# Kernel tuning notes

Measured on AMD Instinct MI355X. Metric: run time of the kernel, lower is better.

The kernel has to match this reference:

```python
import jax, jax.numpy as jnp
import numpy as np

NUM_HEADS = 12
DIM = 768
HEAD_DIM = DIM // NUM_HEADS


def setup_inputs() -> dict:
    key = jax.random.key(0)
    k1, k2, k3, k4 = jax.random.split(key, 4)
    B, N, C = 4, 8192, DIM
    x = jax.random.normal(k1, (B, N, C), dtype=jnp.float32)
    # torch nn.Linear stores weight as (out_features, in_features)
    W_qkv = jax.random.normal(k2, (3 * C, C), dtype=jnp.float32) * (1.0 / np.sqrt(C))
    W_proj = jax.random.normal(k3, (C, C), dtype=jnp.float32) * (1.0 / np.sqrt(C))
    b_proj = jax.random.normal(k4, (C,), dtype=jnp.float32) * 0.01
    return {"x": x, "W_qkv": W_qkv, "W_proj": W_proj, "b_proj": b_proj}


def reference(x, W_qkv, W_proj, b_proj):
    B, N, C = x.shape
    H, D = NUM_HEADS, HEAD_DIM
    qkv = x @ W_qkv.T                                  # [B,N,3C]
    qkv = qkv.reshape(B, N, 3, H, D).transpose(2, 0, 3, 1, 4)  # [3,B,H,N,D]
    q, k, v = qkv[0], qkv[1], qkv[2]
    q = jax.nn.elu(q) + 1.0
    k = jax.nn.elu(k) + 1.0
    k_sum = k.sum(axis=-2)                             # [B,H,D]
    kv = jnp.einsum('bhnd,bhne->bhde', k, v)           # [B,H,D,D]
    numerator = jnp.einsum('bhnd,bhde->bhne', q, kv)   # [B,H,N,D]
    denominator = jnp.einsum('bhnd,bhd->bhn', q, k_sum)
    out = numerator / (denominator[..., None] + 1e-6)
    out = out.transpose(0, 2, 1, 3).reshape(B, N, C)   # [B,N,C]
    out = out @ W_proj.T + b_proj
    return out
```

## Files before the change

kernel.cpp:

```cpp
#include <hip/hip_runtime.h>
#include <hip/hip_bf16.h>
#include <stdint.h>

typedef __attribute__((ext_vector_type(8))) short short8;
typedef __attribute__((ext_vector_type(4))) float floatx4;

#define NB 4
#define NN 8192
#define NC 768
#define NH 12
#define ND 64
#define LDQKV 2304

__device__ __forceinline__ float bf2f(ushort u) {
    union { float f; uint32_t i; } x; x.i = ((uint32_t)u) << 16; return x.f;
}
__device__ __forceinline__ ushort f2bf(float f) {
    union { float f; uint32_t i; } x; x.f = f;
    uint32_t r = x.i + 0x7fff + ((x.i >> 16) & 1);
    return (ushort)(r >> 16);
}
typedef const __attribute__((address_space(1))) uint32_t* gas1_t;
typedef __attribute__((address_space(3))) uint32_t* las3_t;
__device__ __forceinline__ void gl_lds16(const void* g, const void* l) {
    __builtin_amdgcn_global_load_lds((gas1_t)(uintptr_t)g,
                                     (las3_t)(uint32_t)(uintptr_t)l, 16, 0, 0);
}

__global__ __launch_bounds__(256) void cvt_bf16(const float* __restrict__ src,
                                                ushort* __restrict__ dst, int n) {
    const int i = (blockIdx.x * 256 + threadIdx.x) * 8;
    if (i >= n) return;
    const float4 a = *(const float4*)(src + i);
    const float4 b = *(const float4*)(src + i + 4);
    short8 v;
    v[0] = (short)f2bf(a.x); v[1] = (short)f2bf(a.y);
    v[2] = (short)f2bf(a.z); v[3] = (short)f2bf(a.w);
    v[4] = (short)f2bf(b.x); v[5] = (short)f2bf(b.y);
    v[6] = (short)f2bf(b.z); v[7] = (short)f2bf(b.w);
    *(short8*)(dst + i) = v;
}


__device__ __forceinline__ void stage_half(const ushort* __restrict__ src, int row0,
                                           int k0, int K, ushort* dst, int t, int w) {
    const int rsub = t >> 3;
    const int ch = (t & 7) ^ (rsub & 7);
    const ushort* g0 = src + (size_t)(row0 + rsub) * K + k0 + ch * 8;
    gl_lds16(g0,                 dst + w * 512);
    gl_lds16(g0 + (size_t)64 * K, dst + 4096 + w * 512);
}

#define PHASE_SYNC() do {                                        \
    __builtin_amdgcn_s_barrier();                                \
    asm volatile("s_waitcnt lgkmcnt(0)" ::: "memory");           \
    __builtin_amdgcn_sched_barrier(0);                           \
} while (0)

template<int LDC, bool ELU, bool BIAS, typename OutT>
__global__ __launch_bounds__(512) void gemm256(const ushort* __restrict__ A,
                                               const ushort* __restrict__ Bw,
                                               const float* __restrict__ bias,
                                               OutT* __restrict__ Cout, int K) {
    __shared__ __align__(16) ushort SL[2][4][8192];
    const int t = threadIdx.x, w = t >> 6, lane = t & 63;
    const int l16 = lane & 15, quad = lane >> 4;
    const int wm = w >> 2, wn = w & 3;
    const int bro = (wn & 1) * 64;

    const int gx = gridDim.x;
    const int nwg = gx * gridDim.y;
    int bid = blockIdx.y * gx + blockIdx.x;
    bid = (bid & 7) * (nwg >> 3) + (bid >> 3);
    const int m0 = (bid / gx) * 256;
    const int n0 = (bid % gx) * 256;
    const int NT = K >> 6;

    floatx4 acc[8][4] = {};
    short8 af[4][2], b01[2][2], b23[2][2];

    stage_half(Bw, n0,       0,  K, &SL[0][0][0], t, w);
    stage_half(Bw, n0 + 128, 0,  K, &SL[0][1][0], t, w);
    stage_half(A,  m0,       0,  K, &SL[0][2][0], t, w);
    stage_half(A,  m0 + 128, 0,  K, &SL[0][3][0], t, w);
    stage_half(Bw, n0,       64, K, &SL[1][0][0], t, w);
    stage_half(Bw, n0 + 128, 64, K, &SL[1][1][0], t, w);
    asm volatile("s_waitcnt vmcnt(4)" ::: "memory");
    __builtin_amdgcn_s_barrier();

    for (int j = 0; j < NT; j++) {
        const int buf = j & 1;
        const ushort* As = &SL[buf][2 + wm][0];
        const ushort* Bs = &SL[buf][wn >> 1][0];

        #pragma unroll
        for (int mi = 0; mi < 4; mi++) {
            const int row = mi * 16 + l16;
            const int sw = (row & 7) << 3;
            const int base = row * 64 + quad * 8;
            af[mi][0] = *(const short8*)&As[base ^ sw];
            af[mi][1] = *(const short8*)&As[(base + 32) ^ sw];
        }
        #pragma unroll
        for (int ni = 0; ni < 2; ni++) {
            const int row = bro + ni * 16 + l16;
            const int sw = (row & 7) << 3;
            const int base = row * 64 + quad * 8;
            b01[ni][0] = *(const short8*)&Bs[base ^ sw];
            b01[ni][1] = *(const short8*)&Bs[(base + 32) ^ sw];
        }
        if (j + 1 < NT) stage_half(A, m0, (j + 1) * 64, K, &SL[buf ^ 1][2][0], t, w);
        PHASE_SYNC();
        __builtin_amdgcn_s_setprio(1);
        #pragma unroll
        for (int mi = 0; mi < 4; mi++)
            #pragma unroll
            for (int ni = 0; ni < 2; ni++) {
                acc[mi][ni] = __builtin_amdgcn_mfma_f32_16x16x32_bf16(af[mi][0], b01[ni][0], acc[mi][ni], 0, 0, 0);
                acc[mi][ni] = __builtin_amdgcn_mfma_f32_16x16x32_bf16(af[mi][1], b01[ni][1], acc[mi][ni], 0, 0, 0);
            }
        __builtin_amdgcn_s_setprio(0);
        __builtin_amdgcn_s_barrier();

        #pragma unroll
        for (int ni = 0; ni < 2; ni++) {
            const int row = bro + (2 + ni) * 16 + l16;
            const int sw = (row & 7) << 3;
            const int base = row * 64 + quad * 8;
            b23[ni][0] = *(const short8*)&Bs[base ^ sw];
            b23[ni][1] = *(const short8*)&Bs[(base + 32) ^ sw];
        }
        if (j + 1 < NT) stage_half(A, m0 + 128, (j + 1) * 64, K, &SL[buf ^ 1][3][0], t, w);
        PHASE_SYNC();
        __builtin_amdgcn_s_setprio(1);
        #pragma unroll
        for (int mi = 0; mi < 4; mi++)
            #pragma unroll
            for (int ni = 0; ni < 2; ni++) {
                acc[mi][2 + ni] = __builtin_amdgcn_mfma_f32_16x16x32_bf16(af[mi][0], b23[ni][0], acc[mi][2 + ni], 0, 0, 0);
                acc[mi][2 + ni] = __builtin_amdgcn_mfma_f32_16x16x32_bf16(af[mi][1], b23[ni][1], acc[mi][2 + ni], 0, 0, 0);
            }
        __builtin_amdgcn_s_setprio(0);
        __builtin_amdgcn_s_barrier();

        #pragma unroll
        for (int mi = 0; mi < 4; mi++) {
            const int row = (4 + mi) * 16 + l16;
            const int sw = (row & 7) << 3;
            const int base = row * 64 + quad * 8;
            af[mi][0] = *(const short8*)&As[base ^ sw];
            af[mi][1] = *(const short8*)&As[(base + 32) ^ sw];
        }
        if (j + 2 < NT) stage_half(Bw, n0, (j + 2) * 64, K, &SL[buf][0][0], t, w);
        PHASE_SYNC();
        __builtin_amdgcn_s_setprio(1);
        #pragma unroll
        for (int mi = 0; mi < 4; mi++)
            #pragma unroll
            for (int ni = 0; ni < 2; ni++) {
                acc[4 + mi][ni] = __builtin_amdgcn_mfma_f32_16x16x32_bf16(af[mi][0], b01[ni][0], acc[4 + mi][ni], 0, 0, 0);
                acc[4 + mi][ni] = __builtin_amdgcn_mfma_f32_16x16x32_bf16(af[mi][1], b01[ni][1], acc[4 + mi][ni], 0, 0, 0);
            }
        __builtin_amdgcn_s_setprio(0);
        __builtin_amdgcn_s_barrier();

        if (j + 2 < NT) stage_half(Bw, n0 + 128, (j + 2) * 64, K, &SL[buf][1][0], t, w);
        __builtin_amdgcn_s_barrier();
        __builtin_amdgcn_s_setprio(1);
        #pragma unroll
        for (int mi = 0; mi < 4; mi++)
            #pragma unroll
            for (int ni = 0; ni < 2; ni++) {
                acc[4 + mi][2 + ni] = __builtin_amdgcn_mfma_f32_16x16x32_bf16(af[mi][0], b23[ni][0], acc[4 + mi][2 + ni], 0, 0, 0);
                acc[4 + mi][2 + ni] = __builtin_amdgcn_mfma_f32_16x16x32_bf16(af[mi][1], b23[ni][1], acc[4 + mi][2 + ni], 0, 0, 0);
            }
        __builtin_amdgcn_s_setprio(0);
        if (j < NT - 2) asm volatile("s_waitcnt vmcnt(4)" ::: "memory");
        else            asm volatile("s_waitcnt vmcnt(0)" ::: "memory");
        __builtin_amdgcn_s_barrier();
    }

    #pragma unroll
    for (int mi = 0; mi < 8; mi++) {
        const int row = m0 + wm * 128 + mi * 16 + quad * 4;
        #pragma unroll
        for (int n = 0; n < 4; n++) {
            const int col = n0 + wn * 64 + n * 16 + l16;
            float bval = 0.f;
            if (BIAS) bval = bias[col];
            #pragma unroll
            for (int r = 0; r < 4; r++) {
                float v = acc[mi][n][r];
                if (ELU) { if (col < 2 * NC) v = (v > 0.f) ? v + 1.f : __expf(v); }
                if (BIAS) v += bval;
                if (sizeof(OutT) == 2) Cout[(size_t)(row + r) * LDC + col] = (OutT)f2bf(v);
                else                   Cout[(size_t)(row + r) * LDC + col] = (OutT)v;
            }
        }
    }
}

__global__ __launch_bounds__(256) void kv_ksum(const ushort* __restrict__ qkv,
                                               float* __restrict__ kvws,
                                               float* __restrict__ ksws) {
    __shared__ ushort klds[128 * 64];
    __shared__ ushort vlds[128 * 64];
    __shared__ float  kvred[64 * 64];
    __shared__ float  ksred[4][64];
    const int bh = blockIdx.y, b = bh / NH, h = bh % NH;
    const int t = threadIdx.x, w = t >> 6, lane = t & 63, l16 = lane & 15, quad = lane >> 4;
    const int n0 = blockIdx.x * 1024;
    const ushort* kbase = qkv + (size_t)(b * NN) * LDQKV + NC     + h * ND;
    const ushort* vbase = qkv + (size_t)(b * NN) * LDQKV + 2 * NC + h * ND;

    floatx4 acc[4][4] = {};
    float ksp = 0.f;
    const int rowT = t >> 3, ch = t & 7;

    for (int s = 0; s < 8; s++) {
        const int nb = n0 + s * 128;
        #pragma unroll
        for (int i = 0; i < 4; i++) {
            const size_t r = (size_t)(nb + i * 32 + rowT) * LDQKV + ch * 8;
            gl_lds16(kbase + r, klds + i * 2048 + w * 512);
            gl_lds16(vbase + r, vlds + i * 2048 + w * 512);
        }
        __syncthreads();
        short8 af[4], bfr[4];
        #pragma unroll
        for (int dt = 0; dt < 4; dt++) {
            short8 v;
            #pragma unroll
            for (int j = 0; j < 8; j++)
                v[j] = (short)klds[(w * 32 + quad * 8 + j) * 64 + dt * 16 + l16];
            af[dt] = v;
        }
        #pragma unroll
        for (int et = 0; et < 4; et++) {
            short8 v;
            #pragma unroll
            for (int j = 0; j < 8; j++)
                v[j] = (short)vlds[(w * 32 + quad * 8 + j) * 64 + et * 16 + l16];
            bfr[et] = v;
        }
        #pragma unroll
        for (int dt = 0; dt < 4; dt++)
            #pragma unroll
            for (int et = 0; et < 4; et++)
                acc[dt][et] = __builtin_amdgcn_mfma_f32_16x16x32_bf16(af[dt], bfr[et], acc[dt][et], 0, 0, 0);
        #pragma unroll
        for (int n = 0; n < 32; n++) ksp += bf2f(klds[(w * 32 + n) * 64 + lane]);
        __syncthreads();
    }

    if (w == 0) {
        #pragma unroll
        for (int dt = 0; dt < 4; dt++)
            #pragma unroll
            for (int et = 0; et < 4; et++)
                #pragma unroll
                for (int r = 0; r < 4; r++)
                    kvred[(dt * 16 + quad * 4 + r) * 64 + et * 16 + l16] = acc[dt][et][r];
    }
    ksred[w][lane] = ksp;
    __syncthreads();
    if (w != 0) {
        #pragma unroll
        for (int dt = 0; dt < 4; dt++)
            #pragma unroll
            for (int et = 0; et < 4; et++)
                #pragma unroll
                for (int r = 0; r < 4; r++)
                    atomicAdd(&kvred[(dt * 16 + quad * 4 + r) * 64 + et * 16 + l16], acc[dt][et][r]);
    }
    __syncthreads();
    for (int i = t; i < 4096; i += 256) atomicAdd(&kvws[(size_t)bh * 4096 + i], kvred[i]);
    if (t < 64) atomicAdd(&ksws[bh * 64 + t], ksred[0][t] + ksred[1][t] + ksred[2][t] + ksred[3][t]);
}

__global__ __launch_bounds__(256) void attn_apply(const ushort* __restrict__ qkv,
                                                  const float* __restrict__ kvws,
                                                  const float* __restrict__ ksws,
                                                  ushort* __restrict__ outpre) {
    __shared__ ushort kvb[64 * 80];
    const int bh = blockIdx.y, b = bh / NH, h = bh % NH;
    const int t = threadIdx.x, w = t >> 6, lane = t & 63, l16 = lane & 15, quad = lane >> 4;

    for (int i = t; i < 4096; i += 256) {
        const int d = i >> 6, e = i & 63;
        kvb[d * 80 + e] = f2bf(kvws[(size_t)bh * 4096 + i]);
    }
    for (int i = t; i < 1024; i += 256) {
        const int d = i >> 4, c = i & 15;
        kvb[d * 80 + 64 + c] = (c == 0) ? f2bf(ksws[bh * 64 + d]) : (ushort)0;
    }
    __syncthreads();

    short8 bfr[5][2];
    #pragma unroll
    for (int et = 0; et < 5; et++)
        #pragma unroll
        for (int ks = 0; ks < 2; ks++) {
            short8 v;
            #pragma unroll
            for (int j = 0; j < 8; j++)
                v[j] = (short)kvb[(ks * 32 + quad * 8 + j) * 80 + et * 16 + l16];
            bfr[et][ks] = v;
        }

    const ushort* qbase = qkv + (size_t)(b * NN) * LDQKV + h * ND;
    ushort* obase = outpre + (size_t)(b * NN) * NC + h * ND;
    const int n0 = blockIdx.x * 1024;

    for (int it = 0; it < 16; it++) {
        const int nt = n0 + (it * 4 + w) * 16;
        const ushort* qp = qbase + (size_t)(nt + l16) * LDQKV + quad * 8;
        const short8 a0 = *(const short8*)qp;
        const short8 a1 = *(const short8*)(qp + 32);
        floatx4 acc[5] = {};
        #pragma unroll
        for (int et = 0; et < 5; et++) {
            acc[et] = __builtin_amdgcn_mfma_f32_16x16x32_bf16(a0, bfr[et][0], acc[et], 0, 0, 0);
            acc[et] = __builtin_amdgcn_mfma_f32_16x16x32_bf16(a1, bfr[et][1], acc[et], 0, 0, 0);
        }
        float dv[4];
        #pragma unroll
        for (int r = 0; r < 4; r++) dv[r] = __shfl(acc[4][r], lane & 48);
        #pragma unroll
        for (int et = 0; et < 4; et++)
            #pragma unroll
            for (int r = 0; r < 4; r++) {
                const float o = acc[et][r] / (dv[r] + 1e-6f);
                obase[(size_t)(nt + quad * 4 + r) * NC + et * 16 + l16] = f2bf(o);
            }
    }
}

__global__ void zero_f32(float* p, int n) {
    const int i = blockIdx.x * 256 + threadIdx.x;
    if (i < n) p[i] = 0.f;
}

extern "C" void kernel_launch(void* const* d_in, const int* in_sizes, int n_in,
                              void* d_out, int out_size, void* d_ws, size_t ws_size,
                              hipStream_t stream) {
    (void)in_sizes; (void)n_in; (void)out_size; (void)ws_size;
    const float* X     = (const float*)d_in[0];
    const float* Wqkv  = (const float*)d_in[1];
    const float* Wproj = (const float*)d_in[2];
    const float* bproj = (const float*)d_in[3];
    float* out = (float*)d_out;

    char* ws = (char*)d_ws;
    size_t off = 0;
    ushort* qkv     = (ushort*)(ws + off); off += (size_t)32768 * 2304 * 2;
    ushort* outpre  = (ushort*)(ws + off); off += (size_t)32768 * 768 * 2;
    ushort* xbf     = (ushort*)(ws + off); off += (size_t)32768 * 768 * 2;
    ushort* wqkvbf  = (ushort*)(ws + off); off += (size_t)2304 * 768 * 2;
    ushort* wprojbf = (ushort*)(ws + off); off += (size_t)768 * 768 * 2;
    float*  kvws    = (float*)(ws + off);  off += (size_t)48 * 4096 * 4;
    float*  ksws    = (float*)(ws + off);

    const int nx = 32768 * 768, nwq = 2304 * 768, nwp = 768 * 768;
    cvt_bf16<<<nx  / (256 * 8), 256, 0, stream>>>(X,     xbf,     nx);
    cvt_bf16<<<nwq / (256 * 8), 256, 0, stream>>>(Wqkv,  wqkvbf,  nwq);
    cvt_bf16<<<nwp / (256 * 8), 256, 0, stream>>>(Wproj, wprojbf, nwp);

    const int nzero = 48 * 4096 + 48 * 64;
    zero_f32<<<(nzero + 255) / 256, 256, 0, stream>>>(kvws, nzero);

    gemm256<LDQKV, true, false, ushort><<<dim3(9, 128), 512, 0, stream>>>(xbf, wqkvbf, nullptr, qkv, NC);
    kv_ksum<<<dim3(8, 48), 256, 0, stream>>>(qkv, kvws, ksws);
    attn_apply<<<dim3(8, 48), 256, 0, stream>>>(qkv, kvws, ksws, outpre);
    gemm256<NC, false, true, float><<<dim3(3, 128), 512, 0, stream>>>(outpre, wprojbf, bproj, out, NC);
}
```

Baseline: 465.2 us.

## Restructure GEMM phase pipeline and replace atomic KV reduction with partials

```diff
diff --git a/kernel.cpp b/kernel.cpp
--- a/kernel.cpp
+++ b/kernel.cpp
@@ -51,12 +51,6 @@
     gl_lds16(g0 + (size_t)64 * K, dst + 4096 + w * 512);
 }
 
-#define PHASE_SYNC() do {                                        \
-    __builtin_amdgcn_s_barrier();                                \
-    asm volatile("s_waitcnt lgkmcnt(0)" ::: "memory");           \
-    __builtin_amdgcn_sched_barrier(0);                           \
-} while (0)
-
 template<int LDC, bool ELU, bool BIAS, typename OutT>
 __global__ __launch_bounds__(512) void gemm256(const ushort* __restrict__ A,
                                                const ushort* __restrict__ Bw,
@@ -77,7 +71,6 @@
     const int NT = K >> 6;
 
     floatx4 acc[8][4] = {};
-    short8 af[4][2], b01[2][2], b23[2][2];
 
     stage_half(Bw, n0,       0,  K, &SL[0][0][0], t, w);
     stage_half(Bw, n0 + 128, 0,  K, &SL[0][1][0], t, w);
@@ -92,14 +85,15 @@
         const int buf = j & 1;
         const ushort* As = &SL[buf][2 + wm][0];
         const ushort* Bs = &SL[buf][wn >> 1][0];
+        short8 afl[4][2], afh[4][2], b01[2][2], b23[2][2];
 
         #pragma unroll
         for (int mi = 0; mi < 4; mi++) {
             const int row = mi * 16 + l16;
             const int sw = (row & 7) << 3;
             const int base = row * 64 + quad * 8;
-            af[mi][0] = *(const short8*)&As[base ^ sw];
-            af[mi][1] = *(const short8*)&As[(base + 32) ^ sw];
+            afl[mi][0] = *(const short8*)&As[base ^ sw];
+            afl[mi][1] = *(const short8*)&As[(base + 32) ^ sw];
         }
         #pragma unroll
         for (int ni = 0; ni < 2; ni++) {
@@ -109,19 +103,6 @@
             b01[ni][0] = *(const short8*)&Bs[base ^ sw];
             b01[ni][1] = *(const short8*)&Bs[(base + 32) ^ sw];
         }
-        if (j + 1 < NT) stage_half(A, m0, (j + 1) * 64, K, &SL[buf ^ 1][2][0], t, w);
-        PHASE_SYNC();
-        __builtin_amdgcn_s_setprio(1);
-        #pragma unroll
-        for (int mi = 0; mi < 4; mi++)
-            #pragma unroll
-            for (int ni = 0; ni < 2; ni++) {
-                acc[mi][ni] = __builtin_amdgcn_mfma_f32_16x16x32_bf16(af[mi][0], b01[ni][0], acc[mi][ni], 0, 0, 0);
-                acc[mi][ni] = __builtin_amdgcn_mfma_f32_16x16x32_bf16(af[mi][1], b01[ni][1], acc[mi][ni], 0, 0, 0);
-            }
-        __builtin_amdgcn_s_setprio(0);
-        __builtin_amdgcn_s_barrier();
-
         #pragma unroll
         for (int ni = 0; ni < 2; ni++) {
             const int row = bro + (2 + ni) * 16 + l16;
@@ -130,15 +111,15 @@
             b23[ni][0] = *(const short8*)&Bs[base ^ sw];
             b23[ni][1] = *(const short8*)&Bs[(base + 32) ^ sw];
         }
-        if (j + 1 < NT) stage_half(A, m0 + 128, (j + 1) * 64, K, &SL[buf ^ 1][3][0], t, w);
-        PHASE_SYNC();
+
+        if (j + 1 < NT) stage_half(A, m0, (j + 1) * 64, K, &SL[buf ^ 1][2][0], t, w);
         __builtin_amdgcn_s_setprio(1);
         #pragma unroll
         for (int mi = 0; mi < 4; mi++)
             #pragma unroll
             for (int ni = 0; ni < 2; ni++) {
-                acc[mi][2 + ni] = __builtin_amdgcn_mfma_f32_16x16x32_bf16(af[mi][0], b23[ni][0], acc[mi][2 + ni], 0, 0, 0);
-                acc[mi][2 + ni] = __builtin_amdgcn_mfma_f32_16x16x32_bf16(af[mi][1], b23[ni][1], acc[mi][2 + ni], 0, 0, 0);
+                acc[mi][ni] = __builtin_amdgcn_mfma_f32_16x16x32_bf16(afl[mi][0], b01[ni][0], acc[mi][ni], 0, 0, 0);
+                acc[mi][ni] = __builtin_amdgcn_mfma_f32_16x16x32_bf16(afl[mi][1], b01[ni][1], acc[mi][ni], 0, 0, 0);
             }
         __builtin_amdgcn_s_setprio(0);
         __builtin_amdgcn_s_barrier();
@@ -148,31 +129,41 @@
             const int row = (4 + mi) * 16 + l16;
             const int sw = (row & 7) << 3;
             const int base = row * 64 + quad * 8;
-            af[mi][0] = *(const short8*)&As[base ^ sw];
-            af[mi][1] = *(const short8*)&As[(base + 32) ^ sw];
-        }
-        if (j + 2 < NT) stage_half(Bw, n0, (j + 2) * 64, K, &SL[buf][0][0], t, w);
-        PHASE_SYNC();
+            afh[mi][0] = *(const short8*)&As[base ^ sw];
+            afh[mi][1] = *(const short8*)&As[(base + 32) ^ sw];
+        }
+        if (j + 1 < NT) stage_half(A, m0 + 128, (j + 1) * 64, K, &SL[buf ^ 1][3][0], t, w);
         __builtin_amdgcn_s_setprio(1);
         #pragma unroll
         for (int mi = 0; mi < 4; mi++)
             #pragma unroll
             for (int ni = 0; ni < 2; ni++) {
-                acc[4 + mi][ni] = __builtin_amdgcn_mfma_f32_16x16x32_bf16(af[mi][0], b01[ni][0], acc[4 + mi][ni], 0, 0, 0);
-                acc[4 + mi][ni] = __builtin_amdgcn_mfma_f32_16x16x32_bf16(af[mi][1], b01[ni][1], acc[4 + mi][ni], 0, 0, 0);
+                acc[mi][2 + ni] = __builtin_amdgcn_mfma_f32_16x16x32_bf16(afl[mi][0], b23[ni][0], acc[mi][2 + ni], 0, 0, 0);
+                acc[mi][2 + ni] = __builtin_amdgcn_mfma_f32_16x16x32_bf16(afl[mi][1], b23[ni][1], acc[mi][2 + ni], 0, 0, 0);
             }
         __builtin_amdgcn_s_setprio(0);
         __builtin_amdgcn_s_barrier();
 
+        if (j + 2 < NT) stage_half(Bw, n0, (j + 2) * 64, K, &SL[buf][0][0], t, w);
+        __builtin_amdgcn_s_setprio(1);
+        #pragma unroll
+        for (int mi = 0; mi < 4; mi++)
+            #pragma unroll
+            for (int ni = 0; ni < 2; ni++) {
+                acc[4 + mi][ni] = __builtin_amdgcn_mfma_f32_16x16x32_bf16(afh[mi][0], b01[ni][0], acc[4 + mi][ni], 0, 0, 0);
+                acc[4 + mi][ni] = __builtin_amdgcn_mfma_f32_16x16x32_bf16(afh[mi][1], b01[ni][1], acc[4 + mi][ni], 0, 0, 0);
+            }
+        __builtin_amdgcn_s_setprio(0);
+        __builtin_amdgcn_s_barrier();
+
         if (j + 2 < NT) stage_half(Bw, n0 + 128, (j + 2) * 64, K, &SL[buf][1][0], t, w);
-        __builtin_amdgcn_s_barrier();
         __builtin_amdgcn_s_setprio(1);
         #pragma unroll
         for (int mi = 0; mi < 4; mi++)
             #pragma unroll
             for (int ni = 0; ni < 2; ni++) {
-                acc[4 + mi][2 + ni] = __builtin_amdgcn_mfma_f32_16x16x32_bf16(af[mi][0], b23[ni][0], acc[4 + mi][2 + ni], 0, 0, 0);
-                acc[4 + mi][2 + ni] = __builtin_amdgcn_mfma_f32_16x16x32_bf16(af[mi][1], b23[ni][1], acc[4 + mi][2 + ni], 0, 0, 0);
+                acc[4 + mi][2 + ni] = __builtin_amdgcn_mfma_f32_16x16x32_bf16(afh[mi][0], b23[ni][0], acc[4 + mi][2 + ni], 0, 0, 0);
+                acc[4 + mi][2 + ni] = __builtin_amdgcn_mfma_f32_16x16x32_bf16(afh[mi][1], b23[ni][1], acc[4 + mi][2 + ni], 0, 0, 0);
             }
         __builtin_amdgcn_s_setprio(0);
         if (j < NT - 2) asm volatile("s_waitcnt vmcnt(4)" ::: "memory");
@@ -201,12 +192,12 @@
 }
 
 __global__ __launch_bounds__(256) void kv_ksum(const ushort* __restrict__ qkv,
-                                               float* __restrict__ kvws,
-                                               float* __restrict__ ksws) {
-    __shared__ ushort klds[128 * 64];
-    __shared__ ushort vlds[128 * 64];
-    __shared__ float  kvred[64 * 64];
+                                               float* __restrict__ kv_part,
+                                               float* __restrict__ ks_part) {
+    __shared__ ushort kvsh[2][128 * 64];
     __shared__ float  ksred[4][64];
+    ushort* klds = kvsh[0];
+    ushort* vlds = kvsh[1];
     const int bh = blockIdx.y, b = bh / NH, h = bh % NH;
     const int t = threadIdx.x, w = t >> 6, lane = t & 63, l16 = lane & 15, quad = lane >> 4;
     const int n0 = blockIdx.x * 1024;
@@ -214,7 +205,10 @@
     const ushort* vbase = qkv + (size_t)(b * NN) * LDQKV + 2 * NC + h * ND;
 
     floatx4 acc[4][4] = {};
-    float ksp = 0.f;
+    floatx4 aks[4] = {};
+    short8 bones;
+    #pragma unroll
+    for (int j = 0; j < 8; j++) bones[j] = (short)0x3F80;
     const int rowT = t >> 3, ch = t & 7;
 
     for (int s = 0; s < 8; s++) {
@@ -244,55 +238,94 @@
             bfr[et] = v;
         }
         #pragma unroll
-        for (int dt = 0; dt < 4; dt++)
+        for (int dt = 0; dt < 4; dt++) {
             #pragma unroll
             for (int et = 0; et < 4; et++)
                 acc[dt][et] = __builtin_amdgcn_mfma_f32_16x16x32_bf16(af[dt], bfr[et], acc[dt][et], 0, 0, 0);
-        #pragma unroll
-        for (int n = 0; n < 32; n++) ksp += bf2f(klds[(w * 32 + n) * 64 + lane]);
+            aks[dt] = __builtin_amdgcn_mfma_f32_16x16x32_bf16(af[dt], bones, aks[dt], 0, 0, 0);
+        }
         __syncthreads();
     }
 
-    if (w == 0) {
+    if (l16 == 0) {
+        #pragma unroll
+        for (int dt = 0; dt < 4; dt++)
+            #pragma unroll
+            for (int r = 0; r < 4; r++)
+                ksred[w][dt * 16 + quad * 4 + r] = aks[dt][r];
+    }
+
+    float* scratch = (float*)kvsh;
+    if (w >= 2) {
+        float* dst = scratch + (w - 2) * 4096;
         #pragma unroll
         for (int dt = 0; dt < 4; dt++)
             #pragma unroll
             for (int et = 0; et < 4; et++)
                 #pragma unroll
                 for (int r = 0; r < 4; r++)
-                    kvred[(dt * 16 + quad * 4 + r) * 64 + et * 16 + l16] = acc[dt][et][r];
-    }
-    ksred[w][lane] = ksp;
+                    dst[(dt * 16 + quad * 4 + r) * 64 + et * 16 + l16] = acc[dt][et][r];
+    }
     __syncthreads();
-    if (w != 0) {
+    if (w < 2) {
+        const float* srcp = scratch + w * 4096;
         #pragma unroll
         for (int dt = 0; dt < 4; dt++)
             #pragma unroll
             for (int et = 0; et < 4; et++)
                 #pragma unroll
                 for (int r = 0; r < 4; r++)
-                    atomicAdd(&kvred[(dt * 16 + quad * 4 + r) * 64 + et * 16 + l16], acc[dt][et][r]);
+                    acc[dt][et][r] += srcp[(dt * 16 + quad * 4 + r) * 64 + et * 16 + l16];
     }
     __syncthreads();
-    for (int i = t; i < 4096; i += 256) atomicAdd(&kvws[(size_t)bh * 4096 + i], kvred[i]);
-    if (t < 64) atomicAdd(&ksws[bh * 64 + t], ksred[0][t] + ksred[1][t] + ksred[2][t] + ksred[3][t]);
+    if (w == 1) {
+        #pragma unroll
+        for (int dt = 0; dt < 4; dt++)
+            #pragma unroll
+            for (int et = 0; et < 4; et++)
+                #pragma unroll
+                for (int r = 0; r < 4; r++)
+                    scratch[(dt * 16 + quad * 4 + r) * 64 + et * 16 + l16] = acc[dt][et][r];
+    }
+    __syncthreads();
+    if (w == 0) {
+        float* outp = kv_part + ((size_t)blockIdx.x * 48 + bh) * 4096;
+        #pragma unroll
+        for (int dt = 0; dt < 4; dt++)
+            #pragma unroll
+            for (int et = 0; et < 4; et++)
+                #pragma unroll
+                for (int r = 0; r < 4; r++) {
+                    const int idx = (dt * 16 + quad * 4 + r) * 64 + et * 16 + l16;
+                    outp[idx] = acc[dt][et][r] + scratch[idx];
+                }
+    }
+    if (t < 64) ks_part[(size_t)blockIdx.x * 48 * 64 + bh * 64 + t] =
+        ksred[0][t] + ksred[1][t] + ksred[2][t] + ksred[3][t];
 }
 
 __global__ __launch_bounds__(256) void attn_apply(const ushort* __restrict__ qkv,
-                                                  const float* __restrict__ kvws,
-                                                  const float* __restrict__ ksws,
+                                                  const float* __restrict__ kv_part,
+                                                  const float* __restrict__ ks_part,
                                                   ushort* __restrict__ outpre) {
     __shared__ ushort kvb[64 * 80];
     const int bh = blockIdx.y, b = bh / NH, h = bh % NH;
     const int t = threadIdx.x, w = t >> 6, lane = t & 63, l16 = lane & 15, quad = lane >> 4;
 
     for (int i = t; i < 4096; i += 256) {
-        const int d = i >> 6, e = i & 63;
-        kvb[d * 80 + e] = f2bf(kvws[(size_t)bh * 4096 + i]);
+        float s = 0.f;
+        #pragma unroll
+        for (int c = 0; c < 8; c++) s += kv_part[((size_t)c * 48 + bh) * 4096 + i];
+        kvb[(i >> 6) * 80 + (i & 63)] = f2bf(s);
     }
     for (int i = t; i < 1024; i += 256) {
         const int d = i >> 4, c = i & 15;
-        kvb[d * 80 + 64 + c] = (c == 0) ? f2bf(ksws[bh * 64 + d]) : (ushort)0;
+        float s = 0.f;
+        if (c == 0) {
+            #pragma unroll
+            for (int cc = 0; cc < 8; cc++) s += ks_part[(size_t)cc * 48 * 64 + bh * 64 + d];
+        }
+        kvb[d * 80 + 64 + c] = (c == 0) ? f2bf(s) : (ushort)0;
     }
     __syncthreads();
 
@@ -334,11 +367,6 @@
                 obase[(size_t)(nt + quad * 4 + r) * NC + et * 16 + l16] = f2bf(o);
             }
     }
-}
-
-__global__ void zero_f32(float* p, int n) {
-    const int i = blockIdx.x * 256 + threadIdx.x;
-    if (i < n) p[i] = 0.f;
 }
 
 extern "C" void kernel_launch(void* const* d_in, const int* in_sizes, int n_in,
@@ -357,20 +385,17 @@
     ushort* outpre  = (ushort*)(ws + off); off += (size_t)32768 * 768 * 2;
     ushort* xbf     = (ushort*)(ws + off); off += (size_t)32768 * 768 * 2;
     ushort* wqkvbf  = (ushort*)(ws + off); off += (size_t)2304 * 768 * 2;
-    ushort* wprojbf = (ushort*)(ws + off); off += (size_t)768 * 768 * 2;
-    float*  kvws    = (float*)(ws + off);  off += (size_t)48 * 4096 * 4;
-    float*  ksws    = (float*)(ws + off);
+    ushort* wprojbf = (ushort*)(ws + off);
+    float* kv_part = (float*)xbf;
+    float* ks_part = kv_part + (size_t)8 * 48 * 4096;
 
     const int nx = 32768 * 768, nwq = 2304 * 768, nwp = 768 * 768;
     cvt_bf16<<<nx  / (256 * 8), 256, 0, stream>>>(X,     xbf,     nx);
     cvt_bf16<<<nwq / (256 * 8), 256, 0, stream>>>(Wqkv,  wqkvbf,  nwq);
     cvt_bf16<<<nwp / (256 * 8), 256, 0, stream>>>(Wproj, wprojbf, nwp);
 
-    const int nzero = 48 * 4096 + 48 * 64;
-    zero_f32<<<(nzero + 255) / 256, 256, 0, stream>>>(kvws, nzero);
-
     gemm256<LDQKV, true, false, ushort><<<dim3(9, 128), 512, 0, stream>>>(xbf, wqkvbf, nullptr, qkv, NC);
-    kv_ksum<<<dim3(8, 48), 256, 0, stream>>>(qkv, kvws, ksws);
-    attn_apply<<<dim3(8, 48), 256, 0, stream>>>(qkv, kvws, ksws, outpre);
+    kv_ksum<<<dim3(8, 48), 256, 0, stream>>>(qkv, kv_part, ks_part);
+    attn_apply<<<dim3(8, 48), 256, 0, stream>>>(qkv, kv_part, ks_part, outpre);
     gemm256<NC, false, true, float><<<dim3(3, 128), 512, 0, stream>>>(outpre, wprojbf, bproj, out, NC);
 }
```

After: 563.9 us. 21.2% more time.
